# Performance work log

Hardware: AMD Instinct MI355X
Metric: run time of the kernel (lower is better)

The kernel has to match this reference:

```python
import jax, jax.numpy as jnp
import numpy as np

B, C, V, L = 32, 32, 207, 128
C_OUT = 32
ORDER = 2


def setup_inputs() -> dict:
    key = jax.random.key(0)
    ks = jax.random.split(key, 6)
    x = jax.random.normal(ks[0], (B, C, V, L), dtype=jnp.float32)
    A0 = jax.random.uniform(ks[1], (V, V), dtype=jnp.float32) / V
    A1 = jax.random.uniform(ks[2], (V, V), dtype=jnp.float32) / V
    A2 = jax.random.uniform(ks[3], (V, V), dtype=jnp.float32) / V
    c_in_total = (ORDER * 3 + 1) * C  # 224
    W = jax.random.normal(ks[4], (C_OUT, c_in_total), dtype=jnp.float32) * 0.05
    b = jax.random.normal(ks[5], (C_OUT,), dtype=jnp.float32) * 0.05
    return {"x": x, "A0": A0, "A1": A1, "A2": A2, "W": W, "b": b}


def _nconv(x, A):
    # x: [n, c, v, l], A: [v, w] -> [n, c, w, l]
    return jnp.einsum('ncvl,vw->ncwl', x, A)


def reference(x, A0, A1, A2, W, b):
    outs = [x]
    for A in (A0, A1, A2):
        x1 = _nconv(x, A)
        outs.append(x1)
        for _ in range(2, ORDER + 1):
            x1 = _nconv(x1, A)
            outs.append(x1)
    h = jnp.concatenate(outs, axis=1)  # [n, 7*C, v, l]
    # 1x1 Conv2d == channel-mixing matmul; dropout is identity in eval mode
    return jnp.einsum('ncvl,oc->novl', h, W) + b[None, :, None, None]
```

## Files before the change

kernel.cpp:

```cpp
#include <hip/hip_runtime.h>

#define VDIM 207
#define LDIM 128
#define VP 224
#define VL (VDIM*LDIM)
#define NC 1024
#define NPOINT (32*VL)
#define APITCH 232

typedef unsigned short u16;
typedef unsigned int u32;
typedef __attribute__((ext_vector_type(4))) float f32x4;
typedef __attribute__((ext_vector_type(8))) short s16x8;

__device__ __forceinline__ u16 f2bf(float f) {
  u32 u = __float_as_uint(f);
  return (u16)((u + 0x7FFFu + ((u >> 16) & 1u)) >> 16);
}
__device__ __forceinline__ float bf2f(u16 h) {
  return __uint_as_float(((u32)h) << 16);
}

__global__ void k_prep(const float* __restrict__ A0, const float* __restrict__ A1,
                       const float* __restrict__ A2, const float* __restrict__ W,
                       u16* __restrict__ AT, float* __restrict__ WT,
                       u16* __restrict__ Wb) {
  int idx = blockIdx.x * 256 + threadIdx.x;
  if (idx < 3 * VP * VP) {
    int i = idx / (VP * VP);
    int r = idx % (VP * VP);
    int w = r / VP, v = r % VP;
    const float* A = (i == 0) ? A0 : ((i == 1) ? A1 : A2);
    float f = (w < VDIM && v < VDIM) ? A[v * VDIM + w] : 0.f;
    AT[idx] = f2bf(f);
  } else {
    int j = idx - 3 * VP * VP;
    if (j < VP * 32) {
      int k = j >> 5, o = j & 31;
      WT[j] = W[o * 224 + k];
    } else if (j < 2 * VP * 32) {
      int j2 = j - VP * 32;
      Wb[j2] = f2bf(W[j2]);
    }
  }
}

__global__ __launch_bounds__(256) void k_xt(const float* __restrict__ x,
                                            u16* __restrict__ xT) {
  __shared__ float tile[64 * 130];
  int nc = blockIdx.x;
  const float* xs = x + (size_t)nc * VL;
  u16* xd = xT + (size_t)nc * (128 * VP);
  int tid = threadIdx.x;
  for (int ch = 0; ch < 4; ++ch) {
    int v0 = ch * 64;
    __syncthreads();
#pragma unroll
    for (int j = 0; j < 8; ++j) {
      int idx = j * 256 + tid;
      int vr = idx >> 5, c4 = idx & 31;
      int v = v0 + vr;
      float4 val = make_float4(0.f, 0.f, 0.f, 0.f);
      if (v < VDIM) val = *(const float4*)(xs + (size_t)v * LDIM + c4 * 4);
      float* trow = &tile[vr * 130 + c4 * 4];
      *(float2*)(trow) = make_float2(val.x, val.y);
      *(float2*)(trow + 2) = make_float2(val.z, val.w);
    }
    __syncthreads();
    int l = tid >> 1, h = tid & 1;
    int vbase = v0 + h * 32;
    if (vbase < VP) {
      u32 wd[16];
#pragma unroll
      for (int j = 0; j < 16; ++j) {
        int v = vbase + 2 * j;
        float f0 = (v < VDIM) ? tile[(h * 32 + 2 * j) * 130 + l] : 0.f;
        float f1 = (v + 1 < VDIM) ? tile[(h * 32 + 2 * j + 1) * 130 + l] : 0.f;
        wd[j] = (u32)f2bf(f0) | ((u32)f2bf(f1) << 16);
      }
      uint4* dst = (uint4*)(xd + (size_t)l * VP + vbase);
#pragma unroll
      for (int t = 0; t < 4; ++t)
        dst[t] = make_uint4(wd[4 * t], wd[4 * t + 1], wd[4 * t + 2], wd[4 * t + 3]);
    }
  }
}

__global__ __launch_bounds__(512, 2) void k_hops(const u16* __restrict__ xT,
                                                 const u16* __restrict__ AT,
                                                 u16* __restrict__ zbuf,
                                                 int i0, int icount) {
  __shared__ __align__(16) u16 smem[208 * APITCH + 128 * APITCH];
  u16* A_s = smem;
  u16* z1T = smem + 208 * APITCH;

  int tid = threadIdx.x;
  int lane = tid & 63, wid = tid >> 6;
  int lane15 = lane & 15, lgrp = lane >> 4;
  int wm = wid >> 2, wn = wid & 3;
  int NMT = 7 - wm;
  int nc = blockIdx.x;
  const u16* xg = xT + (size_t)nc * (128 * VP);

  if (tid < 256) {
    int l = tid >> 1, h = tid & 1;
    *(uint4*)(z1T + l * APITCH + 208 + h * 8) = make_uint4(0, 0, 0, 0);
  }

  int col0 = wn * 32 + lane15;
  int col1 = col0 + 16;

  for (int ii = 0; ii < icount; ++ii) {
    int i = i0 + ii;
    const u16* Ag = AT + i * (VP * VP);
    for (int j = tid; j < 5824; j += 512) {
      int r = j / 28, cq = j - r * 28;
      *(uint4*)(A_s + r * APITCH + cq * 8) =
          *(const uint4*)(Ag + r * VP + cq * 8);
    }
    __syncthreads();

    for (int hop = 0; hop < 2; ++hop) {
      f32x4 acc[14];
#pragma unroll
      for (int m = 0; m < 14; ++m) acc[m] = (f32x4){0.f, 0.f, 0.f, 0.f};

      for (int ks = 0; ks < 7; ++ks) {
        s16x8 b0, b1;
        if (hop == 0) {
          b0 = *(const s16x8*)(xg + (size_t)col0 * VP + ks * 32 + lgrp * 8);
          b1 = *(const s16x8*)(xg + (size_t)col1 * VP + ks * 32 + lgrp * 8);
        } else {
          b0 = *(const s16x8*)(z1T + col0 * APITCH + ks * 32 + lgrp * 8);
          b1 = *(const s16x8*)(z1T + col1 * APITCH + ks * 32 + lgrp * 8);
        }
#pragma unroll
        for (int mt = 0; mt < 7; ++mt) {
          if (mt < NMT) {
            int row = wm * 112 + mt * 16 + lane15;
            s16x8 afrag = *(const s16x8*)(A_s + row * APITCH + ks * 32 + lgrp * 8);
            asm("v_mfma_f32_16x16x32_bf16 %0, %1, %2, %0"
                : "+v"(acc[mt * 2 + 0])
                : "v"(afrag), "v"(b0));
            asm("v_mfma_f32_16x16x32_bf16 %0, %1, %2, %0"
                : "+v"(acc[mt * 2 + 1])
                : "v"(afrag), "v"(b1));
          }
        }
      }

      if (hop == 1) __syncthreads();

      int slot = 2 * ii + hop;
      u16* zg = zbuf + (size_t)slot * ((size_t)NC * VL) + (size_t)nc * VL;
#pragma unroll
      for (int mt = 0; mt < 7; ++mt) {
        if (mt < NMT) {
#pragma unroll
          for (int nt = 0; nt < 2; ++nt) {
            f32x4 a = acc[mt * 2 + nt];
            int col = wn * 32 + nt * 16 + lane15;
            int wb = wm * 112 + mt * 16 + lgrp * 4;
            u16 u0 = f2bf(a.x), u1 = f2bf(a.y), u2 = f2bf(a.z), u3 = f2bf(a.w);
            if (hop == 0) {
              uint2 pk = make_uint2((u32)u0 | ((u32)u1 << 16),
                                    (u32)u2 | ((u32)u3 << 16));
              *(uint2*)(z1T + col * APITCH + wb) = pk;
            }
            if (wb + 0 < VDIM) zg[(wb + 0) * LDIM + col] = u0;
            if (wb + 1 < VDIM) zg[(wb + 1) * LDIM + col] = u1;
            if (wb + 2 < VDIM) zg[(wb + 2) * LDIM + col] = u2;
            if (wb + 3 < VDIM) zg[(wb + 3) * LDIM + col] = u3;
          }
        }
      }
      if (hop == 0) __syncthreads();
    }
  }
}

__global__ __launch_bounds__(256, 2) void k_mixm(const float* __restrict__ x,
                                                 const u16* __restrict__ zb,
                                                 const u16* __restrict__ Wb,
                                                 const float* __restrict__ bias,
                                                 float* __restrict__ out) {
  __shared__ __align__(16) u16 hT_s[128 * APITCH];
  __shared__ __align__(16) u16 tile[32 * 136];
  int tid = threadIdx.x;
  int bid = blockIdx.x;
  int n = bid / 207, pt = bid - n * 207;
  int p0 = pt * 128;
  int lane = tid & 63, wn = tid >> 6;
  int lane15 = lane & 15, lgrp = lane >> 4;

  s16x8 wa0[7], wa1[7];
#pragma unroll
  for (int ks = 0; ks < 7; ++ks) {
    wa0[ks] = *(const s16x8*)(Wb + lane15 * 224 + ks * 32 + lgrp * 8);
    wa1[ks] = *(const s16x8*)(Wb + (16 + lane15) * 224 + ks * 32 + lgrp * 8);
  }

  for (int g7 = 0; g7 < 7; ++g7) {
    if (g7 == 0) {
#pragma unroll
      for (int j0 = 0; j0 < 4; ++j0) {
        int j = j0 * 256 + tid;
        int c = j >> 5, q = j & 31;
        float4 v = *(const float4*)(x + (size_t)(n * 32 + c) * VL + p0 + q * 4);
        u32 lo = (u32)f2bf(v.x) | ((u32)f2bf(v.y) << 16);
        u32 hi = (u32)f2bf(v.z) | ((u32)f2bf(v.w) << 16);
        *(uint2*)(tile + c * 136 + q * 4) = make_uint2(lo, hi);
      }
    } else {
      int g = g7 - 1;
#pragma unroll
      for (int j0 = 0; j0 < 2; ++j0) {
        int j = j0 * 256 + tid;
        int c = j >> 4, cq = j & 15;
        *(uint4*)(tile + c * 136 + cq * 8) =
            *(const uint4*)(zb + ((size_t)(g << 10) + n * 32 + c) * VL + p0 + cq * 8);
      }
    }
    __syncthreads();
#pragma unroll
    for (int j0 = 0; j0 < 8; ++j0) {
      int j = j0 * 256 + tid;
      int cp = j & 15, p = j >> 4;
      u32 w = (u32)tile[(2 * cp) * 136 + p] |
              ((u32)tile[(2 * cp + 1) * 136 + p] << 16);
      *(u32*)(hT_s + p * APITCH + g7 * 32 + 2 * cp) = w;
    }
    __syncthreads();
  }

  f32x4 acc[2][2];
#pragma unroll
  for (int mt = 0; mt < 2; ++mt)
#pragma unroll
    for (int nt = 0; nt < 2; ++nt) acc[mt][nt] = (f32x4){0.f, 0.f, 0.f, 0.f};

#pragma unroll
  for (int ks = 0; ks < 7; ++ks) {
#pragma unroll
    for (int nt = 0; nt < 2; ++nt) {
      int colp = wn * 32 + nt * 16 + lane15;
      s16x8 bfrag = *(const s16x8*)(hT_s + colp * APITCH + ks * 32 + lgrp * 8);
      asm("v_mfma_f32_16x16x32_bf16 %0, %1, %2, %0"
          : "+v"(acc[0][nt]) : "v"(wa0[ks]), "v"(bfrag));
      asm("v_mfma_f32_16x16x32_bf16 %0, %1, %2, %0"
          : "+v"(acc[1][nt]) : "v"(wa1[ks]), "v"(bfrag));
    }
  }

#pragma unroll
  for (int mt = 0; mt < 2; ++mt) {
#pragma unroll
    for (int j = 0; j < 4; ++j) {
      int o = mt * 16 + lgrp * 4 + j;
      float bv = bias[o];
#pragma unroll
      for (int nt = 0; nt < 2; ++nt) {
        int p = p0 + wn * 32 + nt * 16 + lane15;
        out[(size_t)(n * 32 + o) * VL + p] = acc[mt][nt][j] + bv;
      }
    }
  }
}

template <int MODE, int NZ>
__global__ __launch_bounds__(256, 4) void k_mix(const float* __restrict__ x,
                                                const u16* __restrict__ zb,
                                                const float* __restrict__ WT,
                                                const float* __restrict__ bias,
                                                float* __restrict__ out, int wk0) {
  int t = blockIdx.x * 256 + threadIdx.x;
  int pp = t * 2;
  int n = pp / VL;
  int rem = pp - n * VL;
  float* op = out + (size_t)n * 32 * VL + rem;
  f32x4 a0[8], a1[8];

  if (MODE == 0) {
#pragma unroll
    for (int j = 0; j < 8; ++j) {
      f32x4 bv = *(const f32x4*)(bias + 4 * j);
      a0[j] = bv;
      a1[j] = bv;
    }
    const float* xp = x + (size_t)n * 32 * VL + rem;
#pragma unroll
    for (int c0 = 0; c0 < 32; c0 += 4) {
      float2 v[4];
#pragma unroll
      for (int q = 0; q < 4; ++q)
        v[q] = *(const float2*)(xp + (size_t)(c0 + q) * VL);
#pragma unroll
      for (int q = 0; q < 4; ++q) {
        const float* wv = WT + (c0 + q) * 32;
#pragma unroll
        for (int j = 0; j < 8; ++j) {
          f32x4 w4 = *(const f32x4*)(wv + 4 * j);
          a0[j] += w4 * v[q].x;
          a1[j] += w4 * v[q].y;
        }
      }
    }
  } else {
#pragma unroll
    for (int j = 0; j < 8; ++j) {
#pragma unroll
      for (int q = 0; q < 4; ++q) {
        float2 r = *(const float2*)(op + (size_t)(4 * j + q) * VL);
        a0[j][q] = r.x;
        a1[j][q] = r.y;
      }
    }
  }

#pragma unroll 1
  for (int g = 0; g < NZ; ++g) {
    const u16* zp = zb + ((size_t)g * NC + (size_t)n * 32) * VL + rem;
    const float* wg = WT + (wk0 + g * 32) * 32;
#pragma unroll
    for (int c0 = 0; c0 < 32; c0 += 4) {
      u32 zv[4];
#pragma unroll
      for (int q = 0; q < 4; ++q)
        zv[q] = *(const u32*)(zp + (size_t)(c0 + q) * VL);
#pragma unroll
      for (int q = 0; q < 4; ++q) {
        float f0 = bf2f((u16)(zv[q] & 0xFFFFu));
        float f1 = bf2f((u16)(zv[q] >> 16));
        const float* wv = wg + (c0 + q) * 32;
#pragma unroll
        for (int j = 0; j < 8; ++j) {
          f32x4 w4 = *(const f32x4*)(wv + 4 * j);
          a0[j] += w4 * f0;
          a1[j] += w4 * f1;
        }
      }
    }
  }

#pragma unroll
  for (int j = 0; j < 8; ++j) {
#pragma unroll
    for (int q = 0; q < 4; ++q) {
      float2 r;
      r.x = a0[j][q];
      r.y = a1[j][q];
      *(float2*)(op + (size_t)(4 * j + q) * VL) = r;
    }
  }
}

extern "C" void kernel_launch(void* const* d_in, const int* in_sizes, int n_in,
                              void* d_out, int out_size, void* d_ws, size_t ws_size,
                              hipStream_t stream) {
  const float* x = (const float*)d_in[0];
  const float* A0 = (const float*)d_in[1];
  const float* A1 = (const float*)d_in[2];
  const float* A2 = (const float*)d_in[3];
  const float* W = (const float*)d_in[4];
  const float* b = (const float*)d_in[5];
  float* out = (float*)d_out;

  const size_t xT_sz = (size_t)NC * 128 * VP * 2;
  const size_t AT_sz = (size_t)3 * VP * VP * 2;
  const size_t WT_sz = (size_t)VP * 32 * 4;
  const size_t Wb_sz = (size_t)VP * 32 * 2;
  const size_t slot_sz = (size_t)NC * VL * 2;

  char* wp = (char*)d_ws;
  u16* xT = (u16*)wp; wp += (xT_sz + 255) & ~(size_t)255;
  u16* AT = (u16*)wp; wp += (AT_sz + 255) & ~(size_t)255;
  float* WT = (float*)wp; wp += (WT_sz + 255) & ~(size_t)255;
  u16* Wb = (u16*)wp; wp += (Wb_sz + 255) & ~(size_t)255;
  u16* zbuf = (u16*)wp;
  size_t base = (size_t)(wp - (char*)d_ws);
  bool bigws = ws_size >= base + 6 * slot_sz;

  k_prep<<<644, 256, 0, stream>>>(A0, A1, A2, W, AT, WT, Wb);
  k_xt<<<NC, 256, 0, stream>>>(x, xT);
  if (bigws) {
    k_hops<<<NC, 512, 0, stream>>>(xT, AT, zbuf, 0, 3);
    k_mixm<<<32 * 207, 256, 0, stream>>>(x, zbuf, Wb, b, out);
  } else {
    const int mixgrid = NPOINT / 512;
    k_mix<0, 0><<<mixgrid, 256, 0, stream>>>(x, nullptr, WT, b, out, 32);
    for (int i = 0; i < 3; ++i) {
      k_hops<<<NC, 512, 0, stream>>>(xT, AT, zbuf, i, 1);
      k_mix<1, 2><<<mixgrid, 256, 0, stream>>>(nullptr, zbuf, WT, nullptr, out,
                                               (1 + 2 * i) * 32);
    }
  }
}
```

Baseline: 355.1 us.

## Double k_hops block to 1024 threads and XOR-swizzle shared memory rows

k_hops now launches 16 waves per block instead of 8. Each wave owns 3–4 M-tiles instead of up to 7, which rebalances the uneven row split and cuts per-thread accumulator registers. Shared-memory rows of A and z1T get a 464-byte pitch with XOR swizzling on odd rows, meant to avoid LDS bank conflicts on fragment loads. The cost is larger-block synchronisation overhead, and with only 1024 blocks there may be fewer resident blocks per CU.

```diff
diff --git a/kernel.cpp b/kernel.cpp
--- a/kernel.cpp
+++ b/kernel.cpp
@@ -7,6 +7,7 @@
 #define NC 1024
 #define NPOINT (32*VL)
 #define APITCH 232
+#define SWZ(row, colb) ((row) * 464 + ((colb) ^ (((row) & 1) << 5)))
 
 typedef unsigned short u16;
 typedef unsigned int u32;
@@ -86,25 +87,26 @@
   }
 }
 
-__global__ __launch_bounds__(512, 2) void k_hops(const u16* __restrict__ xT,
-                                                 const u16* __restrict__ AT,
-                                                 u16* __restrict__ zbuf,
-                                                 int i0, int icount) {
+__global__ __launch_bounds__(1024, 4) void k_hops(const u16* __restrict__ xT,
+                                                  const u16* __restrict__ AT,
+                                                  u16* __restrict__ zbuf,
+                                                  int i0, int icount) {
   __shared__ __align__(16) u16 smem[208 * APITCH + 128 * APITCH];
-  u16* A_s = smem;
-  u16* z1T = smem + 208 * APITCH;
+  char* A_b = (char*)smem;
+  char* z_b = (char*)(smem + 208 * APITCH);
 
   int tid = threadIdx.x;
   int lane = tid & 63, wid = tid >> 6;
   int lane15 = lane & 15, lgrp = lane >> 4;
   int wm = wid >> 2, wn = wid & 3;
-  int NMT = 7 - wm;
+  int NMT = (wm == 0) ? 4 : 3;
+  int mbase = (wm == 0) ? 0 : (16 + wm * 48);
   int nc = blockIdx.x;
   const u16* xg = xT + (size_t)nc * (128 * VP);
 
   if (tid < 256) {
     int l = tid >> 1, h = tid & 1;
-    *(uint4*)(z1T + l * APITCH + 208 + h * 8) = make_uint4(0, 0, 0, 0);
+    *(uint4*)(z_b + SWZ(l, 416 + 16 * h)) = make_uint4(0, 0, 0, 0);
   }
 
   int col0 = wn * 32 + lane15;
@@ -113,37 +115,39 @@
   for (int ii = 0; ii < icount; ++ii) {
     int i = i0 + ii;
     const u16* Ag = AT + i * (VP * VP);
-    for (int j = tid; j < 5824; j += 512) {
+    for (int j = tid; j < 5824; j += 1024) {
       int r = j / 28, cq = j - r * 28;
-      *(uint4*)(A_s + r * APITCH + cq * 8) =
-          *(const uint4*)(Ag + r * VP + cq * 8);
+      *(uint4*)(A_b + SWZ(r, cq * 16)) = *(const uint4*)(Ag + r * VP + cq * 8);
     }
     __syncthreads();
 
     for (int hop = 0; hop < 2; ++hop) {
-      f32x4 acc[14];
-#pragma unroll
-      for (int m = 0; m < 14; ++m) acc[m] = (f32x4){0.f, 0.f, 0.f, 0.f};
+      f32x4 acc[4][2];
+#pragma unroll
+      for (int m = 0; m < 4; ++m)
+#pragma unroll
+        for (int nt = 0; nt < 2; ++nt) acc[m][nt] = (f32x4){0.f, 0.f, 0.f, 0.f};
 
       for (int ks = 0; ks < 7; ++ks) {
+        int colb = ks * 64 + lgrp * 16;
         s16x8 b0, b1;
         if (hop == 0) {
           b0 = *(const s16x8*)(xg + (size_t)col0 * VP + ks * 32 + lgrp * 8);
           b1 = *(const s16x8*)(xg + (size_t)col1 * VP + ks * 32 + lgrp * 8);
         } else {
-          b0 = *(const s16x8*)(z1T + col0 * APITCH + ks * 32 + lgrp * 8);
-          b1 = *(const s16x8*)(z1T + col1 * APITCH + ks * 32 + lgrp * 8);
+          b0 = *(const s16x8*)(z_b + SWZ(col0, colb));
+          b1 = *(const s16x8*)(z_b + SWZ(col1, colb));
         }
 #pragma unroll
-        for (int mt = 0; mt < 7; ++mt) {
+        for (int mt = 0; mt < 4; ++mt) {
           if (mt < NMT) {
-            int row = wm * 112 + mt * 16 + lane15;
-            s16x8 afrag = *(const s16x8*)(A_s + row * APITCH + ks * 32 + lgrp * 8);
+            int row = mbase + mt * 16 + lane15;
+            s16x8 afrag = *(const s16x8*)(A_b + SWZ(row, colb));
             asm("v_mfma_f32_16x16x32_bf16 %0, %1, %2, %0"
-                : "+v"(acc[mt * 2 + 0])
+                : "+v"(acc[mt][0])
                 : "v"(afrag), "v"(b0));
             asm("v_mfma_f32_16x16x32_bf16 %0, %1, %2, %0"
-                : "+v"(acc[mt * 2 + 1])
+                : "+v"(acc[mt][1])
                 : "v"(afrag), "v"(b1));
           }
         }
@@ -154,18 +158,18 @@
       int slot = 2 * ii + hop;
       u16* zg = zbuf + (size_t)slot * ((size_t)NC * VL) + (size_t)nc * VL;
 #pragma unroll
-      for (int mt = 0; mt < 7; ++mt) {
+      for (int mt = 0; mt < 4; ++mt) {
         if (mt < NMT) {
 #pragma unroll
           for (int nt = 0; nt < 2; ++nt) {
-            f32x4 a = acc[mt * 2 + nt];
+            f32x4 a = acc[mt][nt];
             int col = wn * 32 + nt * 16 + lane15;
-            int wb = wm * 112 + mt * 16 + lgrp * 4;
+            int wb = mbase + mt * 16 + lgrp * 4;
             u16 u0 = f2bf(a.x), u1 = f2bf(a.y), u2 = f2bf(a.z), u3 = f2bf(a.w);
             if (hop == 0) {
               uint2 pk = make_uint2((u32)u0 | ((u32)u1 << 16),
                                     (u32)u2 | ((u32)u3 << 16));
-              *(uint2*)(z1T + col * APITCH + wb) = pk;
+              *(uint2*)(z_b + SWZ(col, wb * 2)) = pk;
             }
             if (wb + 0 < VDIM) zg[(wb + 0) * LDIM + col] = u0;
             if (wb + 1 < VDIM) zg[(wb + 1) * LDIM + col] = u1;
@@ -383,13 +387,13 @@
   k_prep<<<644, 256, 0, stream>>>(A0, A1, A2, W, AT, WT, Wb);
   k_xt<<<NC, 256, 0, stream>>>(x, xT);
   if (bigws) {
-    k_hops<<<NC, 512, 0, stream>>>(xT, AT, zbuf, 0, 3);
+    k_hops<<<NC, 1024, 0, stream>>>(xT, AT, zbuf, 0, 3);
     k_mixm<<<32 * 207, 256, 0, stream>>>(x, zbuf, Wb, b, out);
   } else {
     const int mixgrid = NPOINT / 512;
     k_mix<0, 0><<<mixgrid, 256, 0, stream>>>(x, nullptr, WT, b, out, 32);
     for (int i = 0; i < 3; ++i) {
-      k_hops<<<NC, 512, 0, stream>>>(xT, AT, zbuf, i, 1);
+      k_hops<<<NC, 1024, 0, stream>>>(xT, AT, zbuf, i, 1);
       k_mix<1, 2><<<mixgrid, 256, 0, stream>>>(nullptr, zbuf, WT, nullptr, out,
                                                (1 + 2 * i) * 32);
     }
```

After: 333.2 us. 6.2% less time.
